# Kernel tuning notes

Hardware: AMD Instinct MI355X
Metric: run time of the kernel (lower is better)

Reference implementation:

```python
import jax, jax.numpy as jnp
import numpy as np

N_NODES = 50000
N_EDGES = 1200000
IN_DIM = 256
HID_DIM = 64
OUT_DIM = 2
BN_EPS = 1e-5


def gcn_conv(x, src, dst, W, b, n_nodes):
    # PyG GCNConv: linear transform, add self-loops, symmetric normalization,
    # scatter-add aggregation at the destination node, then bias.
    h = x @ W                                   # [N, d_out]
    loops = jnp.arange(n_nodes, dtype=src.dtype)
    src_all = jnp.concatenate([src, loops])      # [E+N]
    dst_all = jnp.concatenate([dst, loops])      # [E+N]
    ones = jnp.ones(src_all.shape[0], dtype=h.dtype)
    deg = jax.ops.segment_sum(ones, dst_all, num_segments=n_nodes)  # in-degree incl. self-loop
    dinv = jnp.where(deg > 0, jax.lax.rsqrt(deg), 0.0)
    norm = dinv[src_all] * dinv[dst_all]         # [E+N]
    msg = h[src_all] * norm[:, None]             # gather + scale  [E+N, d_out]
    out = jax.ops.segment_sum(msg, dst_all, num_segments=n_nodes)
    return out + b


def setup_inputs() -> dict:
    key = jax.random.key(0)
    k = jax.random.split(key, 8)
    x = jax.random.normal(k[0], (N_NODES, IN_DIM), dtype=jnp.float32)
    edge_index = jax.random.randint(k[1], (2, N_EDGES), 0, N_NODES, dtype=jnp.int32)
    s1 = 1.0 / np.sqrt(IN_DIM)
    s2 = 1.0 / np.sqrt(HID_DIM)
    W1 = jax.random.uniform(k[2], (IN_DIM, HID_DIM), jnp.float32, -s1, s1)
    b1 = jax.random.uniform(k[3], (HID_DIM,), jnp.float32, -s1, s1)
    gamma = jnp.ones((HID_DIM,), jnp.float32)
    beta = jnp.zeros((HID_DIM,), jnp.float32)
    W2 = jax.random.uniform(k[4], (HID_DIM, OUT_DIM), jnp.float32, -s2, s2)
    b2 = jax.random.uniform(k[5], (OUT_DIM,), jnp.float32, -s2, s2)
    return {"x": x, "edge_index": edge_index, "W1": W1, "b1": b1,
            "gamma": gamma, "beta": beta, "W2": W2, "b2": b2}


def reference(x, edge_index, W1, b1, gamma, beta, W2, b2):
    src, dst = edge_index[0], edge_index[1]
    h = gcn_conv(x, src, dst, W1, b1, N_NODES)       # conv1
    # BatchNorm1d over nodes (training-style batch statistics, biased var)
    mean = jnp.mean(h, axis=0)
    var = jnp.mean((h - mean) ** 2, axis=0)
    h = (h - mean) * jax.lax.rsqrt(var + BN_EPS) * gamma + beta
    # Dropout(0.3) treated as identity (eval mode) for determinism
    h = jax.nn.relu(h)
    return gcn_conv(h, src, dst, W2, b2, N_NODES)    # conv2 -> [N, 2]
```

## Files before the change

kernel.cpp:

```cpp
#include <hip/hip_runtime.h>
#include <hip/hip_bf16.h>

#define NODES   50000
#define EDGES   1200000
#define IND     256
#define HID     64
#define BN_EPS  1e-5f
#define BSHIFT  6
#define BNODES  64
#define NBUCK   782
#define EPB     4096
#define BIN_BLOCKS 293
#define BSTRIDE 2560
#define DMAX    64
#define GBLK    782

using bf16x8 = __attribute__((ext_vector_type(8))) short;
using f32x4  = __attribute__((ext_vector_type(4))) float;

static __device__ __forceinline__ unsigned f2bf2(float lo, float hi) {
    __hip_bfloat16 a = __float2bfloat16(lo);
    __hip_bfloat16 b = __float2bfloat16(hi);
    unsigned ua = *reinterpret_cast<unsigned short*>(&a);
    unsigned ub = *reinterpret_cast<unsigned short*>(&b);
    return ua | (ub << 16);
}
static __device__ __forceinline__ float bf_lo(unsigned u) {
    u <<= 16; return *reinterpret_cast<float*>(&u);
}
static __device__ __forceinline__ float bf_hi(unsigned u) {
    u &= 0xFFFF0000u; return *reinterpret_cast<float*>(&u);
}

__global__ __launch_bounds__(256) void k_prep(const float* __restrict__ W1, unsigned short* __restrict__ W1t,
                                              int* cursor, float* bnsum, float* bnsq) {
    int t = threadIdx.x;
    if (blockIdx.x < 16) {
        int id = blockIdx.x * 256 + t;
        int c = id >> 6, k4 = id & 63;
        float v0 = W1[(k4 * 4 + 0) * HID + c];
        float v1 = W1[(k4 * 4 + 1) * HID + c];
        float v2 = W1[(k4 * 4 + 2) * HID + c];
        float v3 = W1[(k4 * 4 + 3) * HID + c];
        uint2 p; p.x = f2bf2(v0, v1); p.y = f2bf2(v2, v3);
        *(uint2*)&W1t[c * 256 + k4 * 4] = p;
    } else {
        for (int j = t; j < NBUCK; j += 256) cursor[j] = 0;
        if (t < HID) { bnsum[t] = 0.f; bnsq[t] = 0.f; }
    }
}

__global__ __launch_bounds__(256) void k_bin(const int* __restrict__ src, const int* __restrict__ dst,
                                             int* cursor, unsigned int* __restrict__ pair_buf) {
    __shared__ int hist[NBUCK];
    __shared__ int base[NBUCK];
    __shared__ int cur[NBUCK];
    int t = threadIdx.x;
    int e0 = blockIdx.x * EPB;
    for (int j = t; j < NBUCK; j += 256) { hist[j] = 0; cur[j] = 0; }
    __syncthreads();
    int d[16];
#pragma unroll
    for (int i = 0; i < 16; ++i) {
        int e = e0 + t + i * 256;
        d[i] = (e < EDGES) ? dst[e] : -1;
        if (d[i] >= 0) atomicAdd(&hist[d[i] >> BSHIFT], 1);
    }
    __syncthreads();
    for (int j = t; j < NBUCK; j += 256) {
        int h = hist[j];
        base[j] = h ? atomicAdd(&cursor[j], h) : 0;
    }
    __syncthreads();
#pragma unroll
    for (int i = 0; i < 16; ++i) {
        int e = e0 + t + i * 256;
        if (d[i] >= 0) {
            int b = d[i] >> BSHIFT;
            int rel = base[b] + atomicAdd(&cur[b], 1);
            if (rel < BSTRIDE)
                pair_buf[b * BSTRIDE + rel] = (unsigned)src[e] | ((unsigned)(d[i] & (BNODES - 1)) << 16);
        }
    }
}

__global__ __launch_bounds__(256) void k_csr(const int* __restrict__ cursor, const unsigned* __restrict__ pair_buf,
                                             unsigned short* __restrict__ csr, unsigned char* __restrict__ deg8,
                                             float* __restrict__ dinv) {
    __shared__ int cur[BNODES];
    int t = threadIdx.x, b = blockIdx.x;
    if (t < BNODES) cur[t] = 0;
    __syncthreads();
    int m = cursor[b]; if (m > BSTRIDE) m = BSTRIDE;
    const unsigned* pb = pair_buf + b * BSTRIDE;
    for (int i = t; i < m; i += 256) {
        unsigned p = pb[i];
        int node = p >> 16;
        int pos = atomicAdd(&cur[node], 1);
        if (pos < DMAX)
            csr[(((b << BSHIFT) + node) << 6) + pos] = (unsigned short)(p & 0xFFFFu);
    }
    __syncthreads();
    if (t < BNODES) {
        int n = (b << BSHIFT) + t;
        if (n < NODES) {
            int c = cur[t]; if (c > DMAX) c = DMAX;
            deg8[n] = (unsigned char)c;
            dinv[n] = rsqrtf((float)(c + 1));
        }
    }
}

__global__ __launch_bounds__(256) void k_gemm1(const float* __restrict__ x, const unsigned short* __restrict__ W1t,
                                               const float* __restrict__ dinv, unsigned short* __restrict__ gb) {
    __shared__ unsigned short xb[64 * 256];
    __shared__ unsigned short wt[64 * 256];
    int t = threadIdx.x, lane = t & 63, w = t >> 6;
    int base = blockIdx.x * 64;
    const float4* x4 = (const float4*)x;

#pragma unroll
    for (int i = 0; i < 16; ++i) {
        int s = i * 256 + t;
        int row = s >> 6, pos = s & 63;
        int rr = base + row; if (rr >= NODES) rr = NODES - 1;
        float4 v = x4[(long)rr * 64 + pos];
        uint2 p; p.x = f2bf2(v.x, v.y); p.y = f2bf2(v.z, v.w);
        *(uint2*)&xb[row * 256 + (((pos >> 1) ^ (row & 7)) << 3) + ((pos & 1) << 2)] = p;
    }
#pragma unroll
    for (int jj = 0; jj < 8; ++jj) {
        int j = w * 8 + jj;
        int row = 2 * j + (lane >> 5);
        int s = (lane & 31) ^ (row & 7);
        const unsigned short* gp = W1t + row * 256 + s * 8;
        __builtin_amdgcn_global_load_lds(
            (const __attribute__((address_space(1))) void*)(unsigned long)(const void*)gp,
            (__attribute__((address_space(3))) void*)(unsigned long)(const void*)(wt + j * 512),
            16, 0, 0);
    }
    asm volatile("s_waitcnt vmcnt(0)" ::: "memory");
    __syncthreads();

    int r = lane & 15, hi = lane >> 4;
    f32x4 acc[4];
#pragma unroll
    for (int ct = 0; ct < 4; ++ct) acc[ct] = f32x4{0.f, 0.f, 0.f, 0.f};

    int m0 = w * 16;
#pragma unroll
    for (int kc = 0; kc < 8; ++kc) {
        bf16x8 a = *(const bf16x8*)&xb[(m0 + r) * 256 + (((kc * 4 + hi) ^ (r & 7)) << 3)];
#pragma unroll
        for (int ct = 0; ct < 4; ++ct) {
            int c = ct * 16 + r;
            bf16x8 b = *(const bf16x8*)&wt[c * 256 + (((kc * 4 + hi) ^ (c & 7)) << 3)];
            acc[ct] = __builtin_amdgcn_mfma_f32_16x16x32_bf16(a, b, acc[ct], 0, 0, 0);
        }
    }

#pragma unroll
    for (int reg = 0; reg < 4; ++reg) {
        int nd = base + m0 + hi * 4 + reg;
        if (nd < NODES) {
            float di = dinv[nd];
#pragma unroll
            for (int ct = 0; ct < 4; ++ct) {
                __hip_bfloat16 hv = __float2bfloat16(acc[ct][reg] * di);
                gb[(long)nd * 64 + ct * 16 + r] = *reinterpret_cast<unsigned short*>(&hv);
            }
        }
    }
}

__global__ __launch_bounds__(256) void k_gather1(const unsigned short* __restrict__ csr,
                                                 const unsigned char* __restrict__ deg8,
                                                 const unsigned* __restrict__ gb, const float* __restrict__ dinv,
                                                 const float* __restrict__ b1, float* __restrict__ h1) {
    int n = (blockIdx.x * 256 + threadIdx.x) >> 6;
    int lane = threadIdx.x & 63;
    if (n >= NODES) return;
    int sub = lane >> 3;
    int c8  = lane & 7;
    const uint4* g4 = (const uint4*)gb;
    float a[8];
#pragma unroll
    for (int i = 0; i < 8; ++i) a[i] = 0.f;
    if (sub == 0) {
        uint4 v = g4[n * 8 + c8];
        a[0] += bf_lo(v.x); a[1] += bf_hi(v.x);
        a[2] += bf_lo(v.y); a[3] += bf_hi(v.y);
        a[4] += bf_lo(v.z); a[5] += bf_hi(v.z);
        a[6] += bf_lo(v.w); a[7] += bf_hi(v.w);
    }
    int cnt = deg8[n];
    const unsigned short* lst = csr + ((long)n << 6);
    int e = sub;
    for (; e + 8 < cnt; e += 16) {
        int sA = lst[e];
        int sB = lst[e + 8];
        uint4 vA = g4[sA * 8 + c8];
        uint4 vB = g4[sB * 8 + c8];
        a[0] += bf_lo(vA.x) + bf_lo(vB.x); a[1] += bf_hi(vA.x) + bf_hi(vB.x);
        a[2] += bf_lo(vA.y) + bf_lo(vB.y); a[3] += bf_hi(vA.y) + bf_hi(vB.y);
        a[4] += bf_lo(vA.z) + bf_lo(vB.z); a[5] += bf_hi(vA.z) + bf_hi(vB.z);
        a[6] += bf_lo(vA.w) + bf_lo(vB.w); a[7] += bf_hi(vA.w) + bf_hi(vB.w);
    }
    for (; e < cnt; e += 8) {
        int s = lst[e];
        uint4 v = g4[s * 8 + c8];
        a[0] += bf_lo(v.x); a[1] += bf_hi(v.x);
        a[2] += bf_lo(v.y); a[3] += bf_hi(v.y);
        a[4] += bf_lo(v.z); a[5] += bf_hi(v.z);
        a[6] += bf_lo(v.w); a[7] += bf_hi(v.w);
    }
#pragma unroll
    for (int off = 8; off <= 32; off <<= 1) {
#pragma unroll
        for (int i = 0; i < 8; ++i) a[i] += __shfl_xor(a[i], off);
    }
    if (sub == 0) {
        float di = dinv[n];
        float4 bb0 = ((const float4*)b1)[c8 * 2];
        float4 bb1 = ((const float4*)b1)[c8 * 2 + 1];
        float4 o0, o1;
        o0.x = fmaf(a[0], di, bb0.x); o0.y = fmaf(a[1], di, bb0.y);
        o0.z = fmaf(a[2], di, bb0.z); o0.w = fmaf(a[3], di, bb0.w);
        o1.x = fmaf(a[4], di, bb1.x); o1.y = fmaf(a[5], di, bb1.y);
        o1.z = fmaf(a[6], di, bb1.z); o1.w = fmaf(a[7], di, bb1.w);
        ((float4*)h1)[n * 16 + c8 * 2] = o0;
        ((float4*)h1)[n * 16 + c8 * 2 + 1] = o1;
    }
}

__global__ __launch_bounds__(256) void k_bnstats(const float* __restrict__ h1, float* bnsum, float* bnsq) {
    __shared__ float sS[256], sQ[256];
    int t = threadIdx.x;
    int j = t & 63;
    int worker = (blockIdx.x * 256 + t) >> 6;
    int nworkers = (gridDim.x * 256) >> 6;
    float s = 0.f, q = 0.f;
    for (int n = worker; n < NODES; n += nworkers) {
        float v = h1[n * HID + j];
        s += v;
        q += v * v;
    }
    sS[t] = s; sQ[t] = q;
    __syncthreads();
    if (t < 64) {
        s = sS[t] + sS[t + 64] + sS[t + 128] + sS[t + 192];
        q = sQ[t] + sQ[t + 64] + sQ[t + 128] + sQ[t + 192];
        atomicAdd(&bnsum[t], s);
        atomicAdd(&bnsq[t], q);
    }
}

__global__ __launch_bounds__(256) void k_q(const float* __restrict__ h1, const float* __restrict__ bnsum,
                                           const float* __restrict__ bnsq, const float* __restrict__ gamma,
                                           const float* __restrict__ beta, const float* __restrict__ W2,
                                           const float* __restrict__ dinv, float* q) {
    int gt = blockIdx.x * 256 + threadIdx.x;
    int lane = threadIdx.x & 63;
    int n = gt >> 6;
    if (n >= NODES) return;
    float mean = bnsum[lane] * (1.f / NODES);
    float var  = bnsq[lane] * (1.f / NODES) - mean * mean;
    float sc = gamma[lane] * rsqrtf(var + BN_EPS);
    float sh = beta[lane] - mean * sc;
    float v = fmaxf(fmaf(h1[n * HID + lane], sc, sh), 0.f);
    float q0 = v * W2[lane * 2 + 0];
    float q1 = v * W2[lane * 2 + 1];
#pragma unroll
    for (int off = 32; off; off >>= 1) {
        q0 += __shfl_down(q0, off);
        q1 += __shfl_down(q1, off);
    }
    if (lane == 0) {
        float di = dinv[n];
        q[n * 2 + 0] = q0 * di;
        q[n * 2 + 1] = q1 * di;
    }
}

__global__ __launch_bounds__(256) void k_gather2(const unsigned short* __restrict__ csr,
                                                 const unsigned char* __restrict__ deg8,
                                                 const float* __restrict__ q, const float* __restrict__ dinv,
                                                 const float* __restrict__ b2, float* __restrict__ out) {
    int gt = blockIdx.x * 256 + threadIdx.x;
    int n = gt >> 2;
    int sub = gt & 3;
    if (n >= NODES) return;
    const float2* q2 = (const float2*)q;
    float q0 = 0.f, q1 = 0.f;
    if (sub == 0) { float2 s = q2[n]; q0 = s.x; q1 = s.y; }
    int cnt = deg8[n];
    const unsigned short* lst = csr + ((long)n << 6);
    int e = sub;
    for (; e + 4 < cnt; e += 8) {
        float2 mA = q2[lst[e]];
        float2 mB = q2[lst[e + 4]];
        q0 += mA.x + mB.x; q1 += mA.y + mB.y;
    }
    for (; e < cnt; e += 4) {
        float2 m = q2[lst[e]];
        q0 += m.x; q1 += m.y;
    }
    q0 += __shfl_xor(q0, 1); q1 += __shfl_xor(q1, 1);
    q0 += __shfl_xor(q0, 2); q1 += __shfl_xor(q1, 2);
    if (sub == 0) {
        float di = dinv[n];
        out[n * 2 + 0] = fmaf(q0, di, b2[0]);
        out[n * 2 + 1] = fmaf(q1, di, b2[1]);
    }
}

extern "C" void kernel_launch(void* const* d_in, const int* in_sizes, int n_in,
                              void* d_out, int out_size, void* d_ws, size_t ws_size,
                              hipStream_t stream) {
    const float* x     = (const float*)d_in[0];
    const int*   ei    = (const int*)d_in[1];
    const float* W1    = (const float*)d_in[2];
    const float* b1    = (const float*)d_in[3];
    const float* gamma = (const float*)d_in[4];
    const float* beta  = (const float*)d_in[5];
    const float* W2    = (const float*)d_in[6];
    const float* b2    = (const float*)d_in[7];
    const int* src = ei;
    const int* dst = ei + EDGES;
    float* out = (float*)d_out;

    char* base = (char*)d_ws;
    float*    dinv = (float*)base;                         base += 50048 * 4;
    unsigned short* gb = (unsigned short*)base;            base += (size_t)50048 * 64 * 2;
    float*    h1   = (float*)base;                         base += (size_t)NODES * HID * 4;
    float*    bnsum = (float*)base;                        base += 64 * 4;
    float*    bnsq  = (float*)base;                        base += 64 * 4;
    int*      cursor = (int*)base;                         base += 1024 * 4;
    unsigned short* csr = (unsigned short*)base;           base += (size_t)50176 * 64 * 2;
    unsigned char*  deg8 = (unsigned char*)base;           base += 50176;
    unsigned short* W1t = (unsigned short*)base;           base += (size_t)64 * 256 * 2;
    unsigned* pair_buf = (unsigned*)h1;
    float*    q = (float*)gb;

    k_prep <<<17, 256, 0, stream>>>(W1, W1t, cursor, bnsum, bnsq);
    k_bin  <<<BIN_BLOCKS, 256, 0, stream>>>(src, dst, cursor, pair_buf);
    k_csr  <<<NBUCK, 256, 0, stream>>>(cursor, pair_buf, csr, deg8, dinv);
    k_gemm1<<<GBLK, 256, 0, stream>>>(x, W1t, dinv, gb);
    k_gather1<<<(NODES * 64) / 256, 256, 0, stream>>>(csr, deg8, (const unsigned*)gb, dinv, b1, h1);
    k_bnstats<<<256, 256, 0, stream>>>(h1, bnsum, bnsq);
    k_q<<<(NODES * 64) / 256, 256, 0, stream>>>(h1, bnsum, bnsq, gamma, beta, W2, dinv, q);
    k_gather2<<<(NODES * 4 + 255) / 256, 256, 0, stream>>>(csr, deg8, q, dinv, b2, out);
}
```

Measured before the change: 117.4 us.

## Stage CSR rows in LDS and split gather1 feature columns across two blocks

k_csr now builds each bucket's 64x64 adjacency slab in shared memory and writes it to global memory with coalesced 16-byte stores, replacing scattered 2-byte global stores. k_gather1 splits the 64 feature columns into two halves handled by separate blocks. Each wavefront then processes 16 edges at once with 4 lanes per half-row instead of 8 edges with 8 lanes, giving more independent gathers in flight per node. The cost is twice as many blocks and reading each neighbor list twice. The slab copy also writes unused slots, which are never read because reads stop at the degree count.

```diff
diff --git a/kernel.cpp b/kernel.cpp
--- a/kernel.cpp
+++ b/kernel.cpp
@@ -87,6 +87,7 @@
 __global__ __launch_bounds__(256) void k_csr(const int* __restrict__ cursor, const unsigned* __restrict__ pair_buf,
                                              unsigned short* __restrict__ csr, unsigned char* __restrict__ deg8,
                                              float* __restrict__ dinv) {
+    __shared__ unsigned short st[BNODES * DMAX];
     __shared__ int cur[BNODES];
     int t = threadIdx.x, b = blockIdx.x;
     if (t < BNODES) cur[t] = 0;
@@ -98,9 +99,13 @@
         int node = p >> 16;
         int pos = atomicAdd(&cur[node], 1);
         if (pos < DMAX)
-            csr[(((b << BSHIFT) + node) << 6) + pos] = (unsigned short)(p & 0xFFFFu);
-    }
-    __syncthreads();
+            st[(node << 6) + pos] = (unsigned short)(p & 0xFFFFu);
+    }
+    __syncthreads();
+    uint4* dst4 = (uint4*)(csr + ((long)b << 12));
+    const uint4* st4 = (const uint4*)st;
+#pragma unroll
+    for (int i = 0; i < 2; ++i) dst4[t + i * 256] = st4[t + i * 256];
     if (t < BNODES) {
         int n = (b << BSHIFT) + t;
         if (n < NODES) {
@@ -177,17 +182,19 @@
                                                  const unsigned char* __restrict__ deg8,
                                                  const unsigned* __restrict__ gb, const float* __restrict__ dinv,
                                                  const float* __restrict__ b1, float* __restrict__ h1) {
-    int n = (blockIdx.x * 256 + threadIdx.x) >> 6;
+    int half = blockIdx.x & 1;
+    int n = (blockIdx.x >> 1) * 4 + (threadIdx.x >> 6);
     int lane = threadIdx.x & 63;
     if (n >= NODES) return;
-    int sub = lane >> 3;
-    int c8  = lane & 7;
+    int sub = lane >> 2;
+    int cg  = lane & 3;
     const uint4* g4 = (const uint4*)gb;
+    int co = half * 4 + cg;
     float a[8];
 #pragma unroll
     for (int i = 0; i < 8; ++i) a[i] = 0.f;
     if (sub == 0) {
-        uint4 v = g4[n * 8 + c8];
+        uint4 v = g4[n * 8 + co];
         a[0] += bf_lo(v.x); a[1] += bf_hi(v.x);
         a[2] += bf_lo(v.y); a[3] += bf_hi(v.y);
         a[4] += bf_lo(v.z); a[5] += bf_hi(v.z);
@@ -196,40 +203,40 @@
     int cnt = deg8[n];
     const unsigned short* lst = csr + ((long)n << 6);
     int e = sub;
-    for (; e + 8 < cnt; e += 16) {
+    for (; e + 16 < cnt; e += 32) {
         int sA = lst[e];
-        int sB = lst[e + 8];
-        uint4 vA = g4[sA * 8 + c8];
-        uint4 vB = g4[sB * 8 + c8];
+        int sB = lst[e + 16];
+        uint4 vA = g4[sA * 8 + co];
+        uint4 vB = g4[sB * 8 + co];
         a[0] += bf_lo(vA.x) + bf_lo(vB.x); a[1] += bf_hi(vA.x) + bf_hi(vB.x);
         a[2] += bf_lo(vA.y) + bf_lo(vB.y); a[3] += bf_hi(vA.y) + bf_hi(vB.y);
         a[4] += bf_lo(vA.z) + bf_lo(vB.z); a[5] += bf_hi(vA.z) + bf_hi(vB.z);
         a[6] += bf_lo(vA.w) + bf_lo(vB.w); a[7] += bf_hi(vA.w) + bf_hi(vB.w);
     }
-    for (; e < cnt; e += 8) {
+    for (; e < cnt; e += 16) {
         int s = lst[e];
-        uint4 v = g4[s * 8 + c8];
+        uint4 v = g4[s * 8 + co];
         a[0] += bf_lo(v.x); a[1] += bf_hi(v.x);
         a[2] += bf_lo(v.y); a[3] += bf_hi(v.y);
         a[4] += bf_lo(v.z); a[5] += bf_hi(v.z);
         a[6] += bf_lo(v.w); a[7] += bf_hi(v.w);
     }
 #pragma unroll
-    for (int off = 8; off <= 32; off <<= 1) {
+    for (int off = 4; off <= 32; off <<= 1) {
 #pragma unroll
         for (int i = 0; i < 8; ++i) a[i] += __shfl_xor(a[i], off);
     }
     if (sub == 0) {
         float di = dinv[n];
-        float4 bb0 = ((const float4*)b1)[c8 * 2];
-        float4 bb1 = ((const float4*)b1)[c8 * 2 + 1];
+        float4 bb0 = ((const float4*)b1)[co * 2];
+        float4 bb1 = ((const float4*)b1)[co * 2 + 1];
         float4 o0, o1;
         o0.x = fmaf(a[0], di, bb0.x); o0.y = fmaf(a[1], di, bb0.y);
         o0.z = fmaf(a[2], di, bb0.z); o0.w = fmaf(a[3], di, bb0.w);
         o1.x = fmaf(a[4], di, bb1.x); o1.y = fmaf(a[5], di, bb1.y);
         o1.z = fmaf(a[6], di, bb1.z); o1.w = fmaf(a[7], di, bb1.w);
-        ((float4*)h1)[n * 16 + c8 * 2] = o0;
-        ((float4*)h1)[n * 16 + c8 * 2 + 1] = o1;
+        ((float4*)h1)[n * 16 + co * 2] = o0;
+        ((float4*)h1)[n * 16 + co * 2 + 1] = o1;
     }
 }
 
@@ -346,7 +353,7 @@
     k_bin  <<<BIN_BLOCKS, 256, 0, stream>>>(src, dst, cursor, pair_buf);
     k_csr  <<<NBUCK, 256, 0, stream>>>(cursor, pair_buf, csr, deg8, dinv);
     k_gemm1<<<GBLK, 256, 0, stream>>>(x, W1t, dinv, gb);
-    k_gather1<<<(NODES * 64) / 256, 256, 0, stream>>>(csr, deg8, (const unsigned*)gb, dinv, b1, h1);
+    k_gather1<<<25000, 256, 0, stream>>>(csr, deg8, (const unsigned*)gb, dinv, b1, h1);
     k_bnstats<<<256, 256, 0, stream>>>(h1, bnsum, bnsq);
     k_q<<<(NODES * 64) / 256, 256, 0, stream>>>(h1, bnsum, bnsq, gamma, beta, W2, dinv, q);
     k_gather2<<<(NODES * 4 + 255) / 256, 256, 0, stream>>>(csr, deg8, q, dinv, b2, out);
```

Result: slower. 134.8 us (+14.8%).
